# Performance work log

Hardware: AMD Instinct MI355X
Metric: run time of the kernel (lower is better)

Reference implementation:

```python
import jax, jax.numpy as jnp
import numpy as np

VOCAB = 256; EMB = 384; D_MODEL = 512; D_INNER = 1024; D_STATE = 16
D_CONV = 4; DT_RANK = 32; NL = 8; B = 2; L = 2048

def silu(x):
    return x * jax.nn.sigmoid(x)

def layernorm(x, g, b):
    mu = x.mean(-1, keepdims=True)
    v = ((x - mu) ** 2).mean(-1, keepdims=True)
    return (x - mu) / jnp.sqrt(v + 1e-5) * g + b

def conv1d_same(x, w, b, pad):
    # x: (B, C, L), w: (O, I, K)
    out = jax.lax.conv_general_dilated(x, w, (1,), [(pad, pad)],
                                       dimension_numbers=('NCH', 'OIH', 'NCH'))
    return out + b[None, :, None]

def mamba_layer(x, in_w, cw, cb, xp_w, dt_w, dt_b, A_log, Dp, out_w):
    # x: (B, L, D_MODEL)
    xz = x @ in_w.T                      # (B, L, 2*D_INNER)
    xi, z = xz[..., :D_INNER], xz[..., D_INNER:]
    # causal depthwise conv over time
    xi_t = xi.transpose(0, 2, 1)         # (B, D_INNER, L)
    xc = jax.lax.conv_general_dilated(xi_t, cw[:, None, :], (1,), [(D_CONV - 1, 0)],
                                      dimension_numbers=('NCH', 'OIH', 'NCH'),
                                      feature_group_count=D_INNER)
    xc = silu(xc + cb[None, :, None]).transpose(0, 2, 1)   # (B, L, D_INNER)
    dbc = xc @ xp_w.T                    # (B, L, DT_RANK + 2*D_STATE)
    dt = jax.nn.softplus(dbc[..., :DT_RANK] @ dt_w.T + dt_b)   # (B, L, D_INNER)
    Bm = dbc[..., DT_RANK:DT_RANK + D_STATE]                    # (B, L, D_STATE)
    Cm = dbc[..., DT_RANK + D_STATE:]                           # (B, L, D_STATE)
    A = -jnp.exp(A_log)                                         # (D_INNER, D_STATE)
    dA = jnp.exp(dt[..., None] * A)                             # (B, L, D_INNER, D_STATE)
    dBx = (dt * xc)[..., None] * Bm[:, :, None, :]              # (B, L, D_INNER, D_STATE)

    def step(h, inp):
        a, bx, c = inp
        h = a * h + bx                                          # (B, D_INNER, D_STATE)
        return h, jnp.einsum('bds,bs->bd', h, c)

    h0 = jnp.zeros((x.shape[0], D_INNER, D_STATE), x.dtype)
    _, ys = jax.lax.scan(step, h0, (dA.transpose(1, 0, 2, 3),
                                    dBx.transpose(1, 0, 2, 3),
                                    Cm.transpose(1, 0, 2)))
    y = ys.transpose(1, 0, 2) + Dp * xc                         # (B, L, D_INNER)
    y = y * silu(z)
    return y @ out_w.T

def setup_inputs() -> dict:
    key = jax.random.key(0)
    ks = jax.random.split(key, 24)
    s = 0.02
    inp = {
        'tokens': jax.random.randint(ks[0], (B, L), 0, VOCAB),
        'emb': jax.random.normal(ks[1], (VOCAB, EMB)) * s,
        'conv1_w': jax.random.normal(ks[2], (512, EMB, 5)) * s,
        'conv1_b': jnp.zeros((512,)),
        'ln1_g': jnp.ones((512,)), 'ln1_b': jnp.zeros((512,)),
        'conv2_w': jax.random.normal(ks[3], (512, 512, 3)) * s,
        'conv2_b': jnp.zeros((512,)),
        'ln2_g': jnp.ones((512,)), 'ln2_b': jnp.zeros((512,)),
        'pos_emb': jax.random.normal(ks[4], (L, D_MODEL)) * s,
        'in_proj_w': jax.random.normal(ks[5], (NL, 2 * D_INNER, D_MODEL)) * s,
        'conv_w': jax.random.normal(ks[6], (NL, D_INNER, D_CONV)) * s,
        'conv_b': jnp.zeros((NL, D_INNER)),
        'x_proj_w': jax.random.normal(ks[7], (NL, DT_RANK + 2 * D_STATE, D_INNER)) * s,
        'dt_proj_w': jax.random.normal(ks[8], (NL, D_INNER, DT_RANK)) * s,
        'dt_proj_b': jnp.full((NL, D_INNER), -4.0),
        'A_log': jnp.log(jnp.tile(jnp.arange(1, D_STATE + 1, dtype=jnp.float32),
                                  (NL, D_INNER, 1))),
        'D': jnp.ones((NL, D_INNER)),
        'out_proj_w': jax.random.normal(ks[9], (NL, D_MODEL, D_INNER)) * s,
        'fc_w': jax.random.normal(ks[10], (VOCAB, D_MODEL)) * s,
        'fc_b': jnp.zeros((VOCAB,)),
    }
    return inp

def reference(tokens, emb, conv1_w, conv1_b, ln1_g, ln1_b, conv2_w, conv2_b,
              ln2_g, ln2_b, pos_emb, in_proj_w, conv_w, conv_b, x_proj_w,
              dt_proj_w, dt_proj_b, A_log, D, out_proj_w, fc_w, fc_b):
    x = emb[tokens]                                   # (B, L, EMB)
    # CNN frontend (GELU + channel LayerNorm, dropout=0 in eval)
    x = x.transpose(0, 2, 1)
    x = jax.nn.gelu(conv1d_same(x, conv1_w, conv1_b, 2), approximate=False)
    x = layernorm(x.transpose(0, 2, 1), ln1_g, ln1_b).transpose(0, 2, 1)
    x = jax.nn.gelu(conv1d_same(x, conv2_w, conv2_b, 1), approximate=False)
    x = layernorm(x.transpose(0, 2, 1), ln2_g, ln2_b)  # (B, L, 512)
    x = x + pos_emb[None, :x.shape[1]]
    for i in range(NL):
        x = mamba_layer(x, in_proj_w[i], conv_w[i], conv_b[i], x_proj_w[i],
                        dt_proj_w[i], dt_proj_b[i], A_log[i], D[i], out_proj_w[i])
    rep = x[:, -1, :]
    return rep @ fc_w.T + fc_b
```

## Files before the change

kernel.cpp:

```cpp
#include <hip/hip_runtime.h>
#include <hip/hip_bf16.h>
#include <math.h>

#define VOCABN 256
#define EMBN   384
#define DM     512
#define DI     1024
#define DSTATE 16
#define DCONVN 4
#define DTRANK 32
#define NLAYER 8
#define BBATCH 2
#define LSEQ   2048
#define MROWS  (BBATCH*LSEQ)
#define SCHUNK 64
#define NCHUNK (LSEQ/SCHUNK)

typedef short s8v  __attribute__((ext_vector_type(8)));
typedef float f32x4 __attribute__((ext_vector_type(4)));

__device__ __forceinline__ ushort f2bf(float f) {
    uint u = __float_as_uint(f);
    return (ushort)((u + 0x7fffu + ((u >> 16) & 1u)) >> 16);
}
__device__ __forceinline__ float bf2f(ushort h) {
    return __uint_as_float((uint)h << 16);
}
__device__ __forceinline__ uint packbf(float f) {
    ushort h = f2bf(f);
    ushort l = f2bf(f - bf2f(h));
    return ((uint)h << 16) | (uint)l;
}
__device__ __forceinline__ void unp4(uint4 p, ushort* hdst, ushort* ldst) {
    ushort4 h, l;
    h.x = (ushort)(p.x >> 16); l.x = (ushort)(p.x & 0xffffu);
    h.y = (ushort)(p.y >> 16); l.y = (ushort)(p.y & 0xffffu);
    h.z = (ushort)(p.z >> 16); l.z = (ushort)(p.z & 0xffffu);
    h.w = (ushort)(p.w >> 16); l.w = (ushort)(p.w & 0xffffu);
    *(ushort4*)hdst = h; *(ushort4*)ldst = l;
}

__global__ void pack4_kernel(const float* __restrict__ a, int na,
                             const float* __restrict__ b, int nb,
                             const float* __restrict__ c, int nc,
                             const float* __restrict__ d, int nd,
                             uint* __restrict__ pa, uint* __restrict__ pb,
                             uint* __restrict__ pc, uint* __restrict__ pd) {
    int i = blockIdx.x * 256 + threadIdx.x;
    if (i < na) pa[i] = packbf(a[i]);
    else if (i < na + nb) pb[i - na] = packbf(b[i - na]);
    else if (i < na + nb + nc) pc[i - na - nb] = packbf(c[i - na - nb]);
    else if (i < na + nb + nc + nd) pd[i - na - nb - nc] = packbf(d[i - na - nb - nc]);
}

template<int CI, int CK>
__global__ void pack_convw_kernel(const float* __restrict__ w, uint* __restrict__ pw) {
    int idx = blockIdx.x * 256 + threadIdx.x;
    if (idx >= 512 * CI * CK) return;
    int k  = idx % CK;
    int ci = (idx / CK) % CI;
    int co = idx / (CK * CI);
    pw[((size_t)(k * 512) + co) * CI + ci] = packbf(w[idx]);
}

__global__ void embed_kernel(const int* __restrict__ tok, const float* __restrict__ emb,
                             uint* __restrict__ px0) {
    int idx = blockIdx.x * 256 + threadIdx.x;
    int c = idx % EMBN;
    int t = idx / EMBN;
    px0[idx] = packbf(emb[tok[t] * EMBN + c]);
}

__device__ __forceinline__ float gelu_exact(float x) {
    return 0.5f * x * (1.f + erff(x * 0.70710678118654752f));
}

template<int CI, int CK, int PAD>
__global__ __launch_bounds__(256) void conv_mfma_kernel(
    const uint* __restrict__ PA, const uint* __restrict__ PW,
    const float* __restrict__ bias, float* __restrict__ out)
{
    constexpr int ROWS = 128 + CK - 1;
    const int t0  = blockIdx.x * 128;
    const int co0 = blockIdx.y * 32;
    const int tid = threadIdx.x;
    const int wid = tid >> 6, lane = tid & 63;
    const int rb = wid * 32;
    const int lr = lane & 15, lk = (lane >> 4) * 8;
    const int bstart = (t0 / LSEQ) * LSEQ;

    __shared__ alignas(16) ushort Ah[ROWS][40], Al[ROWS][40];
    __shared__ alignas(16) ushort Bh[CK][32][40], Bl[CK][32][40];

    f32x4 acc[2][2];
#pragma unroll
    for (int m = 0; m < 2; m++)
#pragma unroll
        for (int n = 0; n < 2; n++) acc[m][n] = (f32x4){0.f, 0.f, 0.f, 0.f};

    for (int ci0 = 0; ci0 < CI; ci0 += 32) {
        __syncthreads();
        for (int idx = tid; idx < ROWS * 8; idx += 256) {
            int r = idx >> 3, c4 = (idx & 7) * 4;
            int g = t0 - PAD + r;
            uint4 v = make_uint4(0u, 0u, 0u, 0u);
            if (g >= bstart && g < bstart + LSEQ)
                v = *(const uint4*)&PA[(size_t)g * CI + ci0 + c4];
            unp4(v, &Ah[r][c4], &Al[r][c4]);
        }
        for (int idx = tid; idx < CK * 32 * 8; idx += 256) {
            int k = idx >> 8;
            int r = (idx >> 3) & 31;
            int c4 = (idx & 7) * 4;
            uint4 v = *(const uint4*)&PW[((size_t)(k * 512) + co0 + r) * CI + ci0 + c4];
            unp4(v, &Bh[k][r][c4], &Bl[k][r][c4]);
        }
        __syncthreads();

#pragma unroll
        for (int k = 0; k < CK; k++) {
            s8v ah[2], al[2], bh[2], bl[2];
#pragma unroll
            for (int m = 0; m < 2; m++) {
                ah[m] = *(const s8v*)&Ah[rb + m * 16 + lr + k][lk];
                al[m] = *(const s8v*)&Al[rb + m * 16 + lr + k][lk];
            }
#pragma unroll
            for (int n = 0; n < 2; n++) {
                bh[n] = *(const s8v*)&Bh[k][n * 16 + lr][lk];
                bl[n] = *(const s8v*)&Bl[k][n * 16 + lr][lk];
            }
#pragma unroll
            for (int m = 0; m < 2; m++)
#pragma unroll
                for (int n = 0; n < 2; n++) {
                    acc[m][n] = __builtin_amdgcn_mfma_f32_16x16x32_bf16(ah[m], bh[n], acc[m][n], 0, 0, 0);
                    acc[m][n] = __builtin_amdgcn_mfma_f32_16x16x32_bf16(ah[m], bl[n], acc[m][n], 0, 0, 0);
                    acc[m][n] = __builtin_amdgcn_mfma_f32_16x16x32_bf16(al[m], bh[n], acc[m][n], 0, 0, 0);
                }
        }
    }

#pragma unroll
    for (int m = 0; m < 2; m++)
#pragma unroll
        for (int n = 0; n < 2; n++) {
            int gcol = co0 + n * 16 + lr;
            float bv = bias[gcol];
#pragma unroll
            for (int r = 0; r < 4; r++) {
                int grow = t0 + rb + m * 16 + (lane >> 4) * 4 + r;
                out[(size_t)grow * 512 + gcol] = gelu_exact(acc[m][n][r] + bv);
            }
        }
}

template<bool ADDPOS, bool PACK>
__global__ __launch_bounds__(256) void ln_kernel(
    const float* __restrict__ in, const float* __restrict__ g, const float* __restrict__ bb,
    const float* __restrict__ pos, float* __restrict__ out, uint* __restrict__ pout)
{
    int row  = blockIdx.x * 4 + (threadIdx.x >> 6);
    int lane = threadIdx.x & 63;
    const float* xr = in + (size_t)row * DM;
    float v[8];
    float s = 0.f;
#pragma unroll
    for (int i = 0; i < 8; i++) { v[i] = xr[lane + i * 64]; s += v[i]; }
#pragma unroll
    for (int o = 32; o >= 1; o >>= 1) s += __shfl_xor(s, o);
    float mu = s * (1.f / 512.f);
    float var = 0.f;
#pragma unroll
    for (int i = 0; i < 8; i++) { float d = v[i] - mu; var = fmaf(d, d, var); }
#pragma unroll
    for (int o = 32; o >= 1; o >>= 1) var += __shfl_xor(var, o);
    var *= (1.f / 512.f);
    float rstd = rsqrtf(var + 1e-5f);
    int t = row & (LSEQ - 1);
#pragma unroll
    for (int i = 0; i < 8; i++) {
        int c = lane + i * 64;
        float o = (v[i] - mu) * rstd * g[c] + bb[c];
        if (ADDPOS) o += pos[t * DM + c];
        if (PACK) pout[(size_t)row * DM + c] = packbf(o);
        else      out [(size_t)row * DM + c] = o;
    }
}

template<int BN, int EPI>
__global__ __launch_bounds__(256) void gemm_mfma_p(
    const uint* __restrict__ PA, int lda,
    const uint* __restrict__ PW,
    const float* __restrict__ bias,
    float* __restrict__ C, uint* __restrict__ PC, int N, int K)
{
    constexpr int MR = (BN == 128) ? 4 : 2;
    constexpr int NR = 4;
    const int m0 = blockIdx.x * 128;
    const int n0 = blockIdx.y * BN;
    const int tid = threadIdx.x;
    const int wid = tid >> 6;
    const int lane = tid & 63;
    const int rb = (BN == 128) ? (wid >> 1) * 64 : wid * 32;
    const int cb = (BN == 128) ? (wid & 1) * 64 : 0;
    const int lr = lane & 15;
    const int lk = (lane >> 4) * 8;

    __shared__ alignas(16) ushort Ah[128][40], Al[128][40];
    __shared__ alignas(16) ushort Bh[BN][40],  Bl[BN][40];

    f32x4 acc[MR][NR];
#pragma unroll
    for (int m = 0; m < MR; m++)
#pragma unroll
        for (int n = 0; n < NR; n++) acc[m][n] = (f32x4){0.f, 0.f, 0.f, 0.f};

    const int srow = tid >> 3;
    const int scol = (tid & 7) * 4;

    for (int k0 = 0; k0 < K; k0 += 32) {
        uint4 av[4], wv[BN / 32];
#pragma unroll
        for (int i = 0; i < 4; i++)
            av[i] = *(const uint4*)&PA[(size_t)(m0 + srow + 32 * i) * lda + k0 + scol];
#pragma unroll
        for (int i = 0; i < BN / 32; i++)
            wv[i] = *(const uint4*)&PW[(size_t)(n0 + srow + 32 * i) * K + k0 + scol];

        __syncthreads();
#pragma unroll
        for (int i = 0; i < 4; i++)
            unp4(av[i], &Ah[srow + 32 * i][scol], &Al[srow + 32 * i][scol]);
#pragma unroll
        for (int i = 0; i < BN / 32; i++)
            unp4(wv[i], &Bh[srow + 32 * i][scol], &Bl[srow + 32 * i][scol]);
        __syncthreads();

        s8v ah[MR], al[MR], bh[NR], bl[NR];
#pragma unroll
        for (int m = 0; m < MR; m++) {
            ah[m] = *(const s8v*)&Ah[rb + m * 16 + lr][lk];
            al[m] = *(const s8v*)&Al[rb + m * 16 + lr][lk];
        }
#pragma unroll
        for (int n = 0; n < NR; n++) {
            bh[n] = *(const s8v*)&Bh[cb + n * 16 + lr][lk];
            bl[n] = *(const s8v*)&Bl[cb + n * 16 + lr][lk];
        }
#pragma unroll
        for (int m = 0; m < MR; m++)
#pragma unroll
            for (int n = 0; n < NR; n++) {
                acc[m][n] = __builtin_amdgcn_mfma_f32_16x16x32_bf16(ah[m], bh[n], acc[m][n], 0, 0, 0);
                acc[m][n] = __builtin_amdgcn_mfma_f32_16x16x32_bf16(ah[m], bl[n], acc[m][n], 0, 0, 0);
                acc[m][n] = __builtin_amdgcn_mfma_f32_16x16x32_bf16(al[m], bh[n], acc[m][n], 0, 0, 0);
            }
    }

#pragma unroll
    for (int m = 0; m < MR; m++)
#pragma unroll
        for (int n = 0; n < NR; n++) {
#pragma unroll
            for (int r = 0; r < 4; r++) {
                int grow = m0 + rb + m * 16 + (lane >> 4) * 4 + r;
                int gcol = n0 + cb + n * 16 + lr;
                float v = acc[m][n][r];
                if (EPI == 3) {
                    v += bias[gcol];
                    v = fmaxf(v, 0.f) + log1pf(expf(-fabsf(v)));
                }
                C[(size_t)grow * N + gcol] = v;
                if (EPI == 2) PC[(size_t)grow * N + gcol] = packbf(v);
            }
        }
}

__global__ void dwconv_silu_kernel(const float* __restrict__ xz, const float* __restrict__ cw,
                                   const float* __restrict__ cb, float* __restrict__ xc,
                                   uint* __restrict__ pxc) {
    int idx = blockIdx.x * 256 + threadIdx.x;
    int d = idx & (DI - 1);
    int r = idx >> 10;
    int tl = r & (LSEQ - 1);
    float acc = cb[d];
#pragma unroll
    for (int k = 0; k < DCONVN; k++) {
        int ts = tl - 3 + k;
        if (ts >= 0) acc = fmaf(xz[(size_t)(r - 3 + k) * (2 * DI) + d], cw[d * DCONVN + k], acc);
    }
    float sig = 1.f / (1.f + expf(-acc));
    float v = acc * sig;
    xc[idx] = v;
    pxc[idx] = packbf(v);
}

__global__ __launch_bounds__(256) void scan_local_kernel(
    const float* __restrict__ dt, const float* __restrict__ xc,
    const float* __restrict__ dbc, const float* __restrict__ A_log,
    float* __restrict__ S, float* __restrict__ P)
{
    const int sg = threadIdx.x & 3;
    const int dl = threadIdx.x >> 2;
    const int dq = blockIdx.x & 15;
    const int c  = (blockIdx.x >> 4) & (NCHUNK - 1);
    const int b  = blockIdx.x >> 9;
    const int d0 = dq * 64;
    const int d  = d0 + dl;
    const int rowbase = b * LSEQ + c * SCHUNK;

    __shared__ float dtl[SCHUNK][68];
    __shared__ float xcl[SCHUNK][68];
    __shared__ float bl [SCHUNK][16];

    for (int i = threadIdx.x; i < SCHUNK * 16; i += 256) {
        int t = i >> 4, c4 = (i & 15) * 4;
        *(float4*)&dtl[t][c4] = *(const float4*)&dt[(size_t)(rowbase + t) * DI + d0 + c4];
        *(float4*)&xcl[t][c4] = *(const float4*)&xc[(size_t)(rowbase + t) * DI + d0 + c4];
    }
    for (int i = threadIdx.x; i < SCHUNK * 4; i += 256) {
        int t = i >> 2, c4 = (i & 3) * 4;
        *(float4*)&bl[t][c4] = *(const float4*)&dbc[(size_t)(rowbase + t) * 64 + DTRANK + c4];
    }

    float4 alog = *(const float4*)&A_log[d * DSTATE + sg * 4];
    float Av[4];
    Av[0] = -expf(alog.x) * 1.44269504f;
    Av[1] = -expf(alog.y) * 1.44269504f;
    Av[2] = -expf(alog.z) * 1.44269504f;
    Av[3] = -expf(alog.w) * 1.44269504f;

    float h[4] = {0.f, 0.f, 0.f, 0.f};
    float sumdt = 0.f;
    __syncthreads();

#pragma unroll 4
    for (int t = 0; t < SCHUNK; t++) {
        float dtv = dtl[t][dl];
        float xcv = xcl[t][dl];
        float4 Bv = *(const float4*)&bl[t][sg * 4];
        float dx = dtv * xcv;
        h[0] = fmaf(exp2f(dtv * Av[0]), h[0], dx * Bv.x);
        h[1] = fmaf(exp2f(dtv * Av[1]), h[1], dx * Bv.y);
        h[2] = fmaf(exp2f(dtv * Av[2]), h[2], dx * Bv.z);
        h[3] = fmaf(exp2f(dtv * Av[3]), h[3], dx * Bv.w);
        sumdt += dtv;
    }
    size_t off = ((size_t)(b * NCHUNK + c) * DI + d) * DSTATE + sg * 4;
    *(float4*)&S[off] = make_float4(h[0], h[1], h[2], h[3]);
    *(float4*)&P[off] = make_float4(exp2f(Av[0] * sumdt), exp2f(Av[1] * sumdt),
                                    exp2f(Av[2] * sumdt), exp2f(Av[3] * sumdt));
}

__global__ __launch_bounds__(256) void scan_combine_kernel(
    const float* __restrict__ S, const float* __restrict__ P, float* __restrict__ H)
{
    int idx = blockIdx.x * 256 + threadIdx.x;
    int b = idx >> 14;
    int rem = idx & 16383;
    float h = 0.f;
#pragma unroll
    for (int c = 0; c < NCHUNK; c++) {
        size_t off = ((size_t)(b * NCHUNK + c) * DI) * DSTATE + rem;
        H[off] = h;
        h = fmaf(P[off], h, S[off]);
    }
}

__global__ __launch_bounds__(256) void scan_out_kernel(
    const float* __restrict__ dt, const float* __restrict__ xc,
    const float* __restrict__ dbc, const float* __restrict__ xz,
    const float* __restrict__ A_log, const float* __restrict__ Dp,
    const float* __restrict__ H, uint* __restrict__ py)
{
    const int sg = threadIdx.x & 3;
    const int dl = threadIdx.x >> 2;
    const int dq = blockIdx.x & 15;
    const int c  = (blockIdx.x >> 4) & (NCHUNK - 1);
    const int b  = blockIdx.x >> 9;
    const int d0 = dq * 64;
    const int d  = d0 + dl;
    const int rowbase = b * LSEQ + c * SCHUNK;

    __shared__ float dtl[SCHUNK][68];
    __shared__ float xcl[SCHUNK][68];
    __shared__ float bcl[SCHUNK][32];

    for (int i = threadIdx.x; i < SCHUNK * 16; i += 256) {
        int t = i >> 4, c4 = (i & 15) * 4;
        *(float4*)&dtl[t][c4] = *(const float4*)&dt[(size_t)(rowbase + t) * DI + d0 + c4];
        *(float4*)&xcl[t][c4] = *(const float4*)&xc[(size_t)(rowbase + t) * DI + d0 + c4];
    }
    for (int i = threadIdx.x; i < SCHUNK * 8; i += 256) {
        int t = i >> 3, c4 = (i & 7) * 4;
        *(float4*)&bcl[t][c4] = *(const float4*)&dbc[(size_t)(rowbase + t) * 64 + DTRANK + c4];
    }

    float4 alog = *(const float4*)&A_log[d * DSTATE + sg * 4];
    float Av[4];
    Av[0] = -expf(alog.x) * 1.44269504f;
    Av[1] = -expf(alog.y) * 1.44269504f;
    Av[2] = -expf(alog.z) * 1.44269504f;
    Av[3] = -expf(alog.w) * 1.44269504f;
    float Dval = Dp[d];

    float4 hv = *(const float4*)&H[((size_t)(b * NCHUNK + c) * DI + d) * DSTATE + sg * 4];
    float h[4] = {hv.x, hv.y, hv.z, hv.w};
    __syncthreads();

#pragma unroll 4
    for (int t = 0; t < SCHUNK; t++) {
        float dtv = dtl[t][dl];
        float xcv = xcl[t][dl];
        float4 Bv = *(const float4*)&bcl[t][sg * 4];
        float4 Cv = *(const float4*)&bcl[t][16 + sg * 4];
        float dx = dtv * xcv;
        h[0] = fmaf(exp2f(dtv * Av[0]), h[0], dx * Bv.x);
        h[1] = fmaf(exp2f(dtv * Av[1]), h[1], dx * Bv.y);
        h[2] = fmaf(exp2f(dtv * Av[2]), h[2], dx * Bv.z);
        h[3] = fmaf(exp2f(dtv * Av[3]), h[3], dx * Bv.w);
        float p = h[0] * Cv.x;
        p = fmaf(h[1], Cv.y, p);
        p = fmaf(h[2], Cv.z, p);
        p = fmaf(h[3], Cv.w, p);
        p += __shfl_xor(p, 1);
        p += __shfl_xor(p, 2);
        if (sg == 0) {
            float zv = xz[(size_t)(rowbase + t) * (2 * DI) + DI + d];
            float zsig = 1.f / (1.f + exp2f(-zv * 1.44269504f));
            py[(size_t)(rowbase + t) * DI + d] = packbf((p + Dval * xcv) * (zv * zsig));
        }
    }
}

__global__ void fc_kernel(const float* __restrict__ x, const float* __restrict__ fcw,
                          const float* __restrict__ fcb, float* __restrict__ out) {
    int b = blockIdx.x;
    int v = threadIdx.x;
    __shared__ float rep[DM];
    const float* xr = x + (size_t)(b * LSEQ + LSEQ - 1) * DM;
    for (int i = threadIdx.x; i < DM; i += 256) rep[i] = xr[i];
    __syncthreads();
    float acc = fcb[v];
    for (int k = 0; k < DM; k++) acc = fmaf(rep[k], fcw[v * DM + k], acc);
    out[b * VOCABN + v] = acc;
}

extern "C" void kernel_launch(void* const* d_in, const int* in_sizes, int n_in,
                              void* d_out, int out_size, void* d_ws, size_t ws_size,
                              hipStream_t stream) {
    const int*   tokens    = (const int*)  d_in[0];
    const float* emb       = (const float*)d_in[1];
    const float* conv1_w   = (const float*)d_in[2];
    const float* conv1_b   = (const float*)d_in[3];
    const float* ln1_g     = (const float*)d_in[4];
    const float* ln1_b     = (const float*)d_in[5];
    const float* conv2_w   = (const float*)d_in[6];
    const float* conv2_b   = (const float*)d_in[7];
    const float* ln2_g     = (const float*)d_in[8];
    const float* ln2_b     = (const float*)d_in[9];
    const float* pos_emb   = (const float*)d_in[10];
    const float* in_proj_w = (const float*)d_in[11];
    const float* conv_w    = (const float*)d_in[12];
    const float* conv_b    = (const float*)d_in[13];
    const float* x_proj_w  = (const float*)d_in[14];
    const float* dt_proj_w = (const float*)d_in[15];
    const float* dt_proj_b = (const float*)d_in[16];
    const float* A_log     = (const float*)d_in[17];
    const float* Dp_all    = (const float*)d_in[18];
    const float* out_proj_w= (const float*)d_in[19];
    const float* fc_w      = (const float*)d_in[20];
    const float* fc_b      = (const float*)d_in[21];

    float* ws = (float*)d_ws;
    float* X    = ws;
    float* T1   = X   + 2097152;
    float* XZ   = T1  + 2097152;
    float* XC   = XZ  + 8388608;
    float* DT   = XC  + 4194304;
    uint*  PY   = (uint*)(DT + 4194304);
    float* DBC  = (float*)PY + 4194304;
    uint*  PX   = (uint*)(DBC + 262144);
    uint*  PXC  = PX  + 2097152;
    uint*  PWIN = PXC + 4194304;
    uint*  PWOUT= PWIN + 1048576;
    uint*  PWX  = PWOUT + 524288;
    uint*  PWDT = PWX + 65536;
    uint*  PDBC = PWDT + 32768;
    uint*  PX0  = (uint*)XZ;
    uint*  PWC1 = (uint*)XC;
    uint*  PWC2 = (uint*)XC + 983040;
    uint*  PB   = (uint*)DT;
    float* SCN_S = (float*)PXC;
    float* SCN_P = SCN_S + 1048576;
    float* SCN_H = SCN_P + 1048576;

    pack_convw_kernel<EMBN, 5><<<(512 * EMBN * 5 + 255) / 256, 256, 0, stream>>>(conv1_w, PWC1);
    pack_convw_kernel<DM,   3><<<(512 * DM   * 3 + 255) / 256, 256, 0, stream>>>(conv2_w, PWC2);
    embed_kernel<<<(MROWS * EMBN) / 256, 256, 0, stream>>>(tokens, emb, PX0);
    conv_mfma_kernel<EMBN, 5, 2><<<dim3(MROWS / 128, 16), 256, 0, stream>>>(PX0, PWC1, conv1_b, T1);
    ln_kernel<false, true><<<MROWS / 4, 256, 0, stream>>>(T1, ln1_g, ln1_b, nullptr, nullptr, PB);
    conv_mfma_kernel<DM, 3, 1><<<dim3(MROWS / 128, 16), 256, 0, stream>>>(PB, PWC2, conv2_b, T1);
    ln_kernel<true, true><<<MROWS / 4, 256, 0, stream>>>(T1, ln2_g, ln2_b, pos_emb, nullptr, PX);

    const int NPACK = 2 * DI * DM + DM * DI + 64 * DI + DI * DTRANK;
    for (int l = 0; l < NLAYER; l++) {
        pack4_kernel<<<(NPACK + 255) / 256, 256, 0, stream>>>(
            in_proj_w + (size_t)l * 2 * DI * DM, 2 * DI * DM,
            out_proj_w + (size_t)l * DM * DI, DM * DI,
            x_proj_w + (size_t)l * 64 * DI, 64 * DI,
            dt_proj_w + (size_t)l * DI * DTRANK, DI * DTRANK,
            PWIN, PWOUT, PWX, PWDT);
        gemm_mfma_p<128, 0><<<dim3(MROWS / 128, (2 * DI) / 128), 256, 0, stream>>>(
            PX, DM, PWIN, nullptr, XZ, nullptr, 2 * DI, DM);
        dwconv_silu_kernel<<<(MROWS * DI) / 256, 256, 0, stream>>>(
            XZ, conv_w + (size_t)l * DI * DCONVN, conv_b + (size_t)l * DI, XC, PXC);
        gemm_mfma_p<64, 2><<<dim3(MROWS / 128, 1), 256, 0, stream>>>(
            PXC, DI, PWX, nullptr, DBC, PDBC, 64, DI);
        gemm_mfma_p<128, 3><<<dim3(MROWS / 128, DI / 128), 256, 0, stream>>>(
            PDBC, 64, PWDT, dt_proj_b + (size_t)l * DI, DT, nullptr, DI, DTRANK);
        scan_local_kernel<<<16 * NCHUNK * BBATCH, 256, 0, stream>>>(
            DT, XC, DBC, A_log + (size_t)l * DI * DSTATE, SCN_S, SCN_P);
        scan_combine_kernel<<<(BBATCH * DI * DSTATE) / 256, 256, 0, stream>>>(
            SCN_S, SCN_P, SCN_H);
        scan_out_kernel<<<16 * NCHUNK * BBATCH, 256, 0, stream>>>(
            DT, XC, DBC, XZ, A_log + (size_t)l * DI * DSTATE, Dp_all + (size_t)l * DI,
            SCN_H, PY);
        gemm_mfma_p<64, 2><<<dim3(MROWS / 128, DM / 64), 256, 0, stream>>>(
            PY, DI, PWOUT, nullptr, X, PX, DM, DI);
    }

    fc_kernel<<<BBATCH, 256, 0, stream>>>(X, fc_w, fc_b, (float*)d_out);
}
```

Measured before the change: 2.300 ms.

## Shrink GEMM and conv tiles, generalize GEMM template, drop LDS staging in scans

The conv kernel tile shrinks from 128 to 64 rows, with warps split across both rows and output channels. The GEMM template is generalized to BM/BN/WM/WN parameters and every projection is launched with 64-row tiles, which doubles the number of blocks. The scan kernels stop staging dt, xc and B/C through shared memory and read them directly from global memory inside the time loop. The aim is more parallelism across the GPU's compute units and less LDS and synchronization overhead, at the cost of less data reuse per tile and uncoalesced per-step global loads in the scans.

```diff
diff --git a/kernel.cpp b/kernel.cpp
--- a/kernel.cpp
+++ b/kernel.cpp
@@ -80,23 +80,22 @@
     const uint* __restrict__ PA, const uint* __restrict__ PW,
     const float* __restrict__ bias, float* __restrict__ out)
 {
-    constexpr int ROWS = 128 + CK - 1;
-    const int t0  = blockIdx.x * 128;
+    constexpr int ROWS = 64 + CK - 1;
+    const int t0  = blockIdx.x * 64;
     const int co0 = blockIdx.y * 32;
     const int tid = threadIdx.x;
     const int wid = tid >> 6, lane = tid & 63;
-    const int rb = wid * 32;
+    const int rb = (wid >> 1) * 32;
+    const int cb = (wid & 1) * 16;
     const int lr = lane & 15, lk = (lane >> 4) * 8;
     const int bstart = (t0 / LSEQ) * LSEQ;
 
     __shared__ alignas(16) ushort Ah[ROWS][40], Al[ROWS][40];
     __shared__ alignas(16) ushort Bh[CK][32][40], Bl[CK][32][40];
 
-    f32x4 acc[2][2];
-#pragma unroll
-    for (int m = 0; m < 2; m++)
-#pragma unroll
-        for (int n = 0; n < 2; n++) acc[m][n] = (f32x4){0.f, 0.f, 0.f, 0.f};
+    f32x4 acc[2];
+#pragma unroll
+    for (int m = 0; m < 2; m++) acc[m] = (f32x4){0.f, 0.f, 0.f, 0.f};
 
     for (int ci0 = 0; ci0 < CI; ci0 += 32) {
         __syncthreads();
@@ -119,40 +118,33 @@
 
 #pragma unroll
         for (int k = 0; k < CK; k++) {
-            s8v ah[2], al[2], bh[2], bl[2];
+            s8v ah[2], al[2], bh, bl;
 #pragma unroll
             for (int m = 0; m < 2; m++) {
                 ah[m] = *(const s8v*)&Ah[rb + m * 16 + lr + k][lk];
                 al[m] = *(const s8v*)&Al[rb + m * 16 + lr + k][lk];
             }
-#pragma unroll
-            for (int n = 0; n < 2; n++) {
-                bh[n] = *(const s8v*)&Bh[k][n * 16 + lr][lk];
-                bl[n] = *(const s8v*)&Bl[k][n * 16 + lr][lk];
+            bh = *(const s8v*)&Bh[k][cb + lr][lk];
+            bl = *(const s8v*)&Bl[k][cb + lr][lk];
+#pragma unroll
+            for (int m = 0; m < 2; m++) {
+                acc[m] = __builtin_amdgcn_mfma_f32_16x16x32_bf16(ah[m], bh, acc[m], 0, 0, 0);
+                acc[m] = __builtin_amdgcn_mfma_f32_16x16x32_bf16(ah[m], bl, acc[m], 0, 0, 0);
+                acc[m] = __builtin_amdgcn_mfma_f32_16x16x32_bf16(al[m], bh, acc[m], 0, 0, 0);
             }
-#pragma unroll
-            for (int m = 0; m < 2; m++)
-#pragma unroll
-                for (int n = 0; n < 2; n++) {
-                    acc[m][n] = __builtin_amdgcn_mfma_f32_16x16x32_bf16(ah[m], bh[n], acc[m][n], 0, 0, 0);
-                    acc[m][n] = __builtin_amdgcn_mfma_f32_16x16x32_bf16(ah[m], bl[n], acc[m][n], 0, 0, 0);
-                    acc[m][n] = __builtin_amdgcn_mfma_f32_16x16x32_bf16(al[m], bh[n], acc[m][n], 0, 0, 0);
-                }
-        }
-    }
-
-#pragma unroll
-    for (int m = 0; m < 2; m++)
-#pragma unroll
-        for (int n = 0; n < 2; n++) {
-            int gcol = co0 + n * 16 + lr;
-            float bv = bias[gcol];
-#pragma unroll
-            for (int r = 0; r < 4; r++) {
-                int grow = t0 + rb + m * 16 + (lane >> 4) * 4 + r;
-                out[(size_t)grow * 512 + gcol] = gelu_exact(acc[m][n][r] + bv);
-            }
-        }
+        }
+    }
+
+    int gcol = co0 + cb + lr;
+    float bv = bias[gcol];
+#pragma unroll
+    for (int m = 0; m < 2; m++) {
+#pragma unroll
+        for (int r = 0; r < 4; r++) {
+            int grow = t0 + rb + m * 16 + (lane >> 4) * 4 + r;
+            out[(size_t)grow * 512 + gcol] = gelu_exact(acc[m][r] + bv);
+        }
+    }
 }
 
 template<bool ADDPOS, bool PACK>
@@ -188,27 +180,28 @@
     }
 }
 
-template<int BN, int EPI>
+template<int BM, int BN, int WM, int WN, int EPI>
 __global__ __launch_bounds__(256) void gemm_mfma_p(
     const uint* __restrict__ PA, int lda,
     const uint* __restrict__ PW,
     const float* __restrict__ bias,
     float* __restrict__ C, uint* __restrict__ PC, int N, int K)
 {
-    constexpr int MR = (BN == 128) ? 4 : 2;
-    constexpr int NR = 4;
-    const int m0 = blockIdx.x * 128;
+    constexpr int MR = BM / WM / 16;
+    constexpr int NR = BN / WN / 16;
+    constexpr int NLOAD = (BM + BN) * 8 / 256;
+    const int m0 = blockIdx.x * BM;
     const int n0 = blockIdx.y * BN;
     const int tid = threadIdx.x;
     const int wid = tid >> 6;
     const int lane = tid & 63;
-    const int rb = (BN == 128) ? (wid >> 1) * 64 : wid * 32;
-    const int cb = (BN == 128) ? (wid & 1) * 64 : 0;
+    const int rb = (wid / WN) * (BM / WM);
+    const int cb = (wid % WN) * (BN / WN);
     const int lr = lane & 15;
     const int lk = (lane >> 4) * 8;
 
-    __shared__ alignas(16) ushort Ah[128][40], Al[128][40];
-    __shared__ alignas(16) ushort Bh[BN][40],  Bl[BN][40];
+    __shared__ alignas(16) ushort Ah[BM][40], Al[BM][40];
+    __shared__ alignas(16) ushort Bh[BN][40], Bl[BN][40];
 
     f32x4 acc[MR][NR];
 #pragma unroll
@@ -216,25 +209,24 @@
 #pragma unroll
         for (int n = 0; n < NR; n++) acc[m][n] = (f32x4){0.f, 0.f, 0.f, 0.f};
 
-    const int srow = tid >> 3;
-    const int scol = (tid & 7) * 4;
-
     for (int k0 = 0; k0 < K; k0 += 32) {
-        uint4 av[4], wv[BN / 32];
-#pragma unroll
-        for (int i = 0; i < 4; i++)
-            av[i] = *(const uint4*)&PA[(size_t)(m0 + srow + 32 * i) * lda + k0 + scol];
-#pragma unroll
-        for (int i = 0; i < BN / 32; i++)
-            wv[i] = *(const uint4*)&PW[(size_t)(n0 + srow + 32 * i) * K + k0 + scol];
-
+        uint4 v[NLOAD];
+#pragma unroll
+        for (int i = 0; i < NLOAD; i++) {
+            int idx = tid + i * 256;
+            int row = idx >> 3, c4 = (idx & 7) * 4;
+            v[i] = (row < BM)
+                 ? *(const uint4*)&PA[(size_t)(m0 + row) * lda + k0 + c4]
+                 : *(const uint4*)&PW[(size_t)(n0 + row - BM) * K + k0 + c4];
+        }
         __syncthreads();
 #pragma unroll
-        for (int i = 0; i < 4; i++)
-            unp4(av[i], &Ah[srow + 32 * i][scol], &Al[srow + 32 * i][scol]);
-#pragma unroll
-        for (int i = 0; i < BN / 32; i++)
-            unp4(wv[i], &Bh[srow + 32 * i][scol], &Bl[srow + 32 * i][scol]);
+        for (int i = 0; i < NLOAD; i++) {
+            int idx = tid + i * 256;
+            int row = idx >> 3, c4 = (idx & 7) * 4;
+            if (row < BM) unp4(v[i], &Ah[row][c4], &Al[row][c4]);
+            else          unp4(v[i], &Bh[row - BM][c4], &Bl[row - BM][c4]);
+        }
         __syncthreads();
 
         s8v ah[MR], al[MR], bh[NR], bl[NR];
@@ -306,23 +298,7 @@
     const int dq = blockIdx.x & 15;
     const int c  = (blockIdx.x >> 4) & (NCHUNK - 1);
     const int b  = blockIdx.x >> 9;
-    const int d0 = dq * 64;
-    const int d  = d0 + dl;
-    const int rowbase = b * LSEQ + c * SCHUNK;
-
-    __shared__ float dtl[SCHUNK][68];
-    __shared__ float xcl[SCHUNK][68];
-    __shared__ float bl [SCHUNK][16];
-
-    for (int i = threadIdx.x; i < SCHUNK * 16; i += 256) {
-        int t = i >> 4, c4 = (i & 15) * 4;
-        *(float4*)&dtl[t][c4] = *(const float4*)&dt[(size_t)(rowbase + t) * DI + d0 + c4];
-        *(float4*)&xcl[t][c4] = *(const float4*)&xc[(size_t)(rowbase + t) * DI + d0 + c4];
-    }
-    for (int i = threadIdx.x; i < SCHUNK * 4; i += 256) {
-        int t = i >> 2, c4 = (i & 3) * 4;
-        *(float4*)&bl[t][c4] = *(const float4*)&dbc[(size_t)(rowbase + t) * 64 + DTRANK + c4];
-    }
+    const int d  = dq * 64 + dl;
 
     float4 alog = *(const float4*)&A_log[d * DSTATE + sg * 4];
     float Av[4];
@@ -333,13 +309,14 @@
 
     float h[4] = {0.f, 0.f, 0.f, 0.f};
     float sumdt = 0.f;
-    __syncthreads();
+    const int rowbase = b * LSEQ + c * SCHUNK;
 
 #pragma unroll 4
     for (int t = 0; t < SCHUNK; t++) {
-        float dtv = dtl[t][dl];
-        float xcv = xcl[t][dl];
-        float4 Bv = *(const float4*)&bl[t][sg * 4];
+        int r = rowbase + t;
+        float dtv = dt[(size_t)r * DI + d];
+        float xcv = xc[(size_t)r * DI + d];
+        float4 Bv = *(const float4*)&dbc[(size_t)r * 64 + DTRANK + sg * 4];
         float dx = dtv * xcv;
         h[0] = fmaf(exp2f(dtv * Av[0]), h[0], dx * Bv.x);
         h[1] = fmaf(exp2f(dtv * Av[1]), h[1], dx * Bv.y);
@@ -379,23 +356,7 @@
     const int dq = blockIdx.x & 15;
     const int c  = (blockIdx.x >> 4) & (NCHUNK - 1);
     const int b  = blockIdx.x >> 9;
-    const int d0 = dq * 64;
-    const int d  = d0 + dl;
-    const int rowbase = b * LSEQ + c * SCHUNK;
-
-    __shared__ float dtl[SCHUNK][68];
-    __shared__ float xcl[SCHUNK][68];
-    __shared__ float bcl[SCHUNK][32];
-
-    for (int i = threadIdx.x; i < SCHUNK * 16; i += 256) {
-        int t = i >> 4, c4 = (i & 15) * 4;
-        *(float4*)&dtl[t][c4] = *(const float4*)&dt[(size_t)(rowbase + t) * DI + d0 + c4];
-        *(float4*)&xcl[t][c4] = *(const float4*)&xc[(size_t)(rowbase + t) * DI + d0 + c4];
-    }
-    for (int i = threadIdx.x; i < SCHUNK * 8; i += 256) {
-        int t = i >> 3, c4 = (i & 7) * 4;
-        *(float4*)&bcl[t][c4] = *(const float4*)&dbc[(size_t)(rowbase + t) * 64 + DTRANK + c4];
-    }
+    const int d  = dq * 64 + dl;
 
     float4 alog = *(const float4*)&A_log[d * DSTATE + sg * 4];
     float Av[4];
@@ -407,14 +368,15 @@
 
     float4 hv = *(const float4*)&H[((size_t)(b * NCHUNK + c) * DI + d) * DSTATE + sg * 4];
     float h[4] = {hv.x, hv.y, hv.z, hv.w};
-    __syncthreads();
-
-#pragma unroll 4
+    const int rowbase = b * LSEQ + c * SCHUNK;
+
+#pragma unroll 2
     for (int t = 0; t < SCHUNK; t++) {
-        float dtv = dtl[t][dl];
-        float xcv = xcl[t][dl];
-        float4 Bv = *(const float4*)&bcl[t][sg * 4];
-        float4 Cv = *(const float4*)&bcl[t][16 + sg * 4];
+        int r = rowbase + t;
+        float dtv = dt[(size_t)r * DI + d];
+        float xcv = xc[(size_t)r * DI + d];
+        float4 Bv = *(const float4*)&dbc[(size_t)r * 64 + DTRANK + sg * 4];
+        float4 Cv = *(const float4*)&dbc[(size_t)r * 64 + DTRANK + DSTATE + sg * 4];
         float dx = dtv * xcv;
         h[0] = fmaf(exp2f(dtv * Av[0]), h[0], dx * Bv.x);
         h[1] = fmaf(exp2f(dtv * Av[1]), h[1], dx * Bv.y);
@@ -427,9 +389,9 @@
         p += __shfl_xor(p, 1);
         p += __shfl_xor(p, 2);
         if (sg == 0) {
-            float zv = xz[(size_t)(rowbase + t) * (2 * DI) + DI + d];
+            float zv = xz[(size_t)r * (2 * DI) + DI + d];
             float zsig = 1.f / (1.f + exp2f(-zv * 1.44269504f));
-            py[(size_t)(rowbase + t) * DI + d] = packbf((p + Dval * xcv) * (zv * zsig));
+            py[(size_t)r * DI + d] = packbf((p + Dval * xcv) * (zv * zsig));
         }
     }
 }
@@ -499,9 +461,9 @@
     pack_convw_kernel<EMBN, 5><<<(512 * EMBN * 5 + 255) / 256, 256, 0, stream>>>(conv1_w, PWC1);
     pack_convw_kernel<DM,   3><<<(512 * DM   * 3 + 255) / 256, 256, 0, stream>>>(conv2_w, PWC2);
     embed_kernel<<<(MROWS * EMBN) / 256, 256, 0, stream>>>(tokens, emb, PX0);
-    conv_mfma_kernel<EMBN, 5, 2><<<dim3(MROWS / 128, 16), 256, 0, stream>>>(PX0, PWC1, conv1_b, T1);
+    conv_mfma_kernel<EMBN, 5, 2><<<dim3(MROWS / 64, 16), 256, 0, stream>>>(PX0, PWC1, conv1_b, T1);
     ln_kernel<false, true><<<MROWS / 4, 256, 0, stream>>>(T1, ln1_g, ln1_b, nullptr, nullptr, PB);
-    conv_mfma_kernel<DM, 3, 1><<<dim3(MROWS / 128, 16), 256, 0, stream>>>(PB, PWC2, conv2_b, T1);
+    conv_mfma_kernel<DM, 3, 1><<<dim3(MROWS / 64, 16), 256, 0, stream>>>(PB, PWC2, conv2_b, T1);
     ln_kernel<true, true><<<MROWS / 4, 256, 0, stream>>>(T1, ln2_g, ln2_b, pos_emb, nullptr, PX);
 
     const int NPACK = 2 * DI * DM + DM * DI + 64 * DI + DI * DTRANK;
@@ -512,13 +474,13 @@
             x_proj_w + (size_t)l * 64 * DI, 64 * DI,
             dt_proj_w + (size_t)l * DI * DTRANK, DI * DTRANK,
             PWIN, PWOUT, PWX, PWDT);
-        gemm_mfma_p<128, 0><<<dim3(MROWS / 128, (2 * DI) / 128), 256, 0, stream>>>(
+        gemm_mfma_p<64, 128, 1, 4, 0><<<dim3(MROWS / 64, (2 * DI) / 128), 256, 0, stream>>>(
             PX, DM, PWIN, nullptr, XZ, nullptr, 2 * DI, DM);
         dwconv_silu_kernel<<<(MROWS * DI) / 256, 256, 0, stream>>>(
             XZ, conv_w + (size_t)l * DI * DCONVN, conv_b + (size_t)l * DI, XC, PXC);
-        gemm_mfma_p<64, 2><<<dim3(MROWS / 128, 1), 256, 0, stream>>>(
+        gemm_mfma_p<64, 64, 2, 2, 2><<<dim3(MROWS / 64, 1), 256, 0, stream>>>(
             PXC, DI, PWX, nullptr, DBC, PDBC, 64, DI);
-        gemm_mfma_p<128, 3><<<dim3(MROWS / 128, DI / 128), 256, 0, stream>>>(
+        gemm_mfma_p<64, 64, 2, 2, 3><<<dim3(MROWS / 64, DI / 64), 256, 0, stream>>>(
             PDBC, 64, PWDT, dt_proj_b + (size_t)l * DI, DT, nullptr, DI, DTRANK);
         scan_local_kernel<<<16 * NCHUNK * BBATCH, 256, 0, stream>>>(
             DT, XC, DBC, A_log + (size_t)l * DI * DSTATE, SCN_S, SCN_P);
@@ -527,7 +489,7 @@
         scan_out_kernel<<<16 * NCHUNK * BBATCH, 256, 0, stream>>>(
             DT, XC, DBC, XZ, A_log + (size_t)l * DI * DSTATE, Dp_all + (size_t)l * DI,
             SCN_H, PY);
-        gemm_mfma_p<64, 2><<<dim3(MROWS / 128, DM / 64), 256, 0, stream>>>(
+        gemm_mfma_p<64, 64, 2, 2, 2><<<dim3(MROWS / 64, DM / 64), 256, 0, stream>>>(
             PY, DI, PWOUT, nullptr, X, PX, DM, DI);
     }
 
```

New measurement: 1.992 ms. 1.16x faster.
